# Kernel optimization log

Measured on AMD Instinct MI355X. Metric: run time of the kernel, lower is better.

The kernel has to match this reference:

```python
import jax, jax.numpy as jnp
import numpy as np

DIM = 512
NUM_HEADS = 16
WINDOW_SIZE = 32
POS_HIDDEN = DIM // 4  # int(dim // mlp_ratio) with mlp_ratio=4.0


def _window_partition(coords, window_size):
    # coords: (B, N, 3) -> window ids (B, N)
    B, N, _ = coords.shape
    cmin = coords.min(axis=1, keepdims=True)
    cmax = coords.max(axis=1, keepdims=True)
    crange = cmax - cmin
    crange = jnp.where(crange < 1e-6, jnp.ones_like(crange), crange)
    cnorm = (coords - cmin) / crange
    grid_res = max(1, round((N / window_size) ** (1.0 / 3.0)))  # static Python int
    bin_idx = jnp.clip((cnorm * grid_res).astype(jnp.int32), 0, grid_res - 1)
    window_id = bin_idx[..., 0] * (grid_res * grid_res) + bin_idx[..., 1] * grid_res + bin_idx[..., 2]
    return window_id


def setup_inputs() -> dict:
    key = jax.random.key(0)
    ks = jax.random.split(key, 10)
    B, N, C = 2, 1024, DIM
    s = 0.02
    return {
        "coords": jax.random.uniform(ks[0], (B, N, 3), dtype=jnp.float32),
        "x": jax.random.normal(ks[1], (B, N, C), dtype=jnp.float32),
        "qkv_w": jax.random.normal(ks[2], (3 * C, C), dtype=jnp.float32) * s,
        "qkv_b": jnp.zeros((3 * C,), dtype=jnp.float32),
        "proj_w": jax.random.normal(ks[3], (C, C), dtype=jnp.float32) * s,
        "proj_b": jnp.zeros((C,), dtype=jnp.float32),
        "pos_w1": jax.random.normal(ks[4], (POS_HIDDEN, 3), dtype=jnp.float32) * 0.1,
        "pos_b1": jnp.zeros((POS_HIDDEN,), dtype=jnp.float32),
        "pos_w2": jax.random.normal(ks[5], (NUM_HEADS, POS_HIDDEN), dtype=jnp.float32) * 0.1,
        "pos_b2": jnp.zeros((NUM_HEADS,), dtype=jnp.float32),
    }


def reference(coords, x, qkv_w, qkv_b, proj_w, proj_b, pos_w1, pos_b1, pos_w2, pos_b2):
    B, N, C = x.shape
    H = NUM_HEADS
    D = C // H
    # QKV projection
    qkv = x @ qkv_w.T + qkv_b  # (B, N, 3C)
    q, k, v = jnp.split(qkv, 3, axis=-1)
    q = q.reshape(B, N, H, D).transpose(0, 2, 1, 3)  # (B, H, N, D)
    k = k.reshape(B, N, H, D).transpose(0, 2, 1, 3)
    v = v.reshape(B, N, H, D).transpose(0, 2, 1, 3)
    window_id = _window_partition(coords, WINDOW_SIZE)  # (B, N)
    scale = D ** (-0.5)
    attn = jnp.einsum("bhnd,bhmd->bhnm", q, k) * scale  # (B, H, N, N)
    # per-pair MLP relative position bias (exact GELU, matching torch nn.GELU)
    offsets = coords[:, :, None, :] - coords[:, None, :, :]  # (B, N, N, 3)
    hid = jax.nn.gelu(offsets @ pos_w1.T + pos_b1, approximate=False)
    rel_pos_bias = hid @ pos_w2.T + pos_b2  # (B, N, N, H)
    attn = attn + rel_pos_bias.transpose(0, 3, 1, 2)
    # window mask: masked_fill with -10000.0 for cross-window pairs
    same_window = (window_id[:, :, None] == window_id[:, None, :])[:, None]  # (B,1,N,N)
    attn = jnp.where(same_window, attn, jnp.float32(-10000.0))
    attn = jax.nn.softmax(attn, axis=-1)
    out = jnp.einsum("bhnm,bhmd->bhnd", attn, v)
    out = out.transpose(0, 2, 1, 3).reshape(B, N, C)
    return out @ proj_w.T + proj_b
```

## Files before the change

### kernel.cpp

```cpp
#include <hip/hip_runtime.h>
#include <hip/hip_bf16.h>
#include <math.h>

#define B_  2
#define N_  1024
#define C_  512
#define H_  16
#define D_  32
#define NW  27
#define NWT (B_*NW)
#define CAPP 98304
#define GEMM_BLKS 768
#define BIAS_BLKS 512

typedef __attribute__((ext_vector_type(8))) short short8;
typedef __attribute__((ext_vector_type(4))) short short4e;
typedef __attribute__((ext_vector_type(4))) float f32x4;

__device__ __forceinline__ ushort f2bf(float x){
  unsigned u = __float_as_uint(x);
  return (ushort)((u + 0x7fffu + ((u>>16)&1u)) >> 16);
}
__device__ __forceinline__ float bf2f(ushort b){
  return __uint_as_float(((unsigned)b)<<16);
}

#define GLL16(gptr, lptr) __builtin_amdgcn_global_load_lds( \
    (const __attribute__((address_space(1))) void*)(gptr),  \
    (__attribute__((address_space(3))) void*)(lptr), 16, 0, 0)

__device__ __forceinline__ float gelu_exact(float t){
  const float y = t*0.70710678118654752f;
  const float u = y*y;
  float E;
  if (u < 0.5f) {
    float q =           -7.5757576e-4f;
    q = fmaf(q,u,  4.6296297e-3f);
    q = fmaf(q,u, -2.3809524e-2f);
    q = fmaf(q,u,  0.1f);
    q = fmaf(q,u, -0.33333334f);
    q = fmaf(q,u,  1.0f);
    E = 1.1283791671f * y * q;
  } else {
    E = erff(y);
  }
  return 0.5f*t*(1.0f + E);
}

__global__ __launch_bounds__(1024) void winprep_kernel(
    const float* __restrict__ coords,
    int* __restrict__ counts, int* __restrict__ offsets, int* __restrict__ sidx,
    const float* __restrict__ x, const float* __restrict__ qkv_w,
    const float* __restrict__ proj_w, const float* __restrict__ pw2,
    const float* __restrict__ pw1, const float* __restrict__ pb1,
    ushort* __restrict__ Xh, ushort* __restrict__ Xl,
    ushort* __restrict__ Wqh, ushort* __restrict__ Wql,
    ushort* __restrict__ Wph, ushort* __restrict__ Wpl,
    ushort* __restrict__ W2bh, ushort* __restrict__ W2bl,
    float4* __restrict__ w14)
{
  const int bid = blockIdx.x;
  if (bid < 2) {
    const int b = bid;
    const int i = threadIdx.x;
    const int lane = i & 63, wv = i >> 6;
    const float c0 = coords[(b*N_+i)*3+0];
    const float c1 = coords[(b*N_+i)*3+1];
    const float c2 = coords[(b*N_+i)*3+2];
    float mn0=c0,mx0=c0,mn1=c1,mx1=c1,mn2=c2,mx2=c2;
    #pragma unroll
    for (int o=32;o>=1;o>>=1) {
      mn0=fminf(mn0,__shfl_xor(mn0,o)); mx0=fmaxf(mx0,__shfl_xor(mx0,o));
      mn1=fminf(mn1,__shfl_xor(mn1,o)); mx1=fmaxf(mx1,__shfl_xor(mx1,o));
      mn2=fminf(mn2,__shfl_xor(mn2,o)); mx2=fmaxf(mx2,__shfl_xor(mx2,o));
    }
    __shared__ float red[16][6];
    __shared__ float bmin[3], rng[3];
    __shared__ int wavecnt[16][NW];
    __shared__ int waveoff[16][NW];
    __shared__ int wcnt[NW], woff[NW];
    if (lane==0){ red[wv][0]=mn0;red[wv][1]=mn1;red[wv][2]=mn2;red[wv][3]=mx0;red[wv][4]=mx1;red[wv][5]=mx2; }
    __syncthreads();
    if (i==0){
      float a0=red[0][0],a1=red[0][1],a2=red[0][2];
      float d0=red[0][3],d1=red[0][4],d2=red[0][5];
      for (int t=1;t<16;++t){
        a0=fminf(a0,red[t][0]); a1=fminf(a1,red[t][1]); a2=fminf(a2,red[t][2]);
        d0=fmaxf(d0,red[t][3]); d1=fmaxf(d1,red[t][4]); d2=fmaxf(d2,red[t][5]);
      }
      bmin[0]=a0;bmin[1]=a1;bmin[2]=a2;
      float r0=d0-a0, r1=d1-a1, r2=d2-a2;
      rng[0]=(r0<1e-6f)?1.f:r0; rng[1]=(r1<1e-6f)?1.f:r1; rng[2]=(r2<1e-6f)?1.f:r2;
    }
    __syncthreads();
    int bx=(int)(((c0-bmin[0])/rng[0])*3.0f); bx=min(max(bx,0),2);
    int by=(int)(((c1-bmin[1])/rng[1])*3.0f); by=min(max(by,0),2);
    int bz=(int)(((c2-bmin[2])/rng[2])*3.0f); bz=min(max(bz,0),2);
    const int wid = bx*9+by*3+bz;
    unsigned long long mymask=0ull;
    for (int w=0;w<NW;++w){
      unsigned long long m = __ballot(wid==w);
      if (w==wid) mymask=m;
      if (lane==0) wavecnt[wv][w]=(int)__popcll(m);
    }
    __syncthreads();
    if (i<NW){ int s=0; for(int t=0;t<16;++t) s+=wavecnt[t][i]; wcnt[i]=s; }
    __syncthreads();
    if (i==0){ int r=0; for(int w=0;w<NW;++w){ woff[w]=r; r+=wcnt[w]; } }
    __syncthreads();
    if (i<NW){ int o=woff[i]; for(int t=0;t<16;++t){ waveoff[t][i]=o; o+=wavecnt[t][i]; } }
    __syncthreads();
    const int rank = waveoff[wv][wid] + (int)__popcll(mymask & ((1ull<<lane)-1ull));
    sidx[b*N_ + rank] = i;
    if (i<NW){ counts[b*NW+i]=wcnt[i]; offsets[b*NW+i]=woff[i]; }
    return;
  }
  const int gid = (bid - 2)*1024 + threadIdx.x;
  if (bid == 2 && threadIdx.x < 128) {
    const int u = threadIdx.x;
    w14[u] = make_float4(pw1[u*3+0], pw1[u*3+1], pw1[u*3+2], pb1[u]);
  }
  if (gid >= 262400) return;
  const float* src; ushort* ph; ushort* pl; int i;
  if (gid < 131072)      { src = x;      ph = Xh;   pl = Xl;   i = gid; }
  else if (gid < 229376) { src = qkv_w;  ph = Wqh;  pl = Wql;  i = gid - 131072; }
  else if (gid < 262144) { src = proj_w; ph = Wph;  pl = Wpl;  i = gid - 229376; }
  else                   { src = pw2;    ph = W2bh; pl = W2bl; i = gid - 262144; }
  const float4 a = ((const float4*)src)[i*2+0];
  const float4 b = ((const float4*)src)[i*2+1];
  const float v[8] = {a.x,a.y,a.z,a.w,b.x,b.y,b.z,b.w};
  ushort hv[8], lv[8];
  #pragma unroll
  for (int t=0;t<8;++t){ hv[t]=f2bf(v[t]); lv[t]=f2bf(v[t]-bf2f(hv[t])); }
  ((ushort4*)ph)[i*2+0] = make_ushort4(hv[0],hv[1],hv[2],hv[3]);
  ((ushort4*)ph)[i*2+1] = make_ushort4(hv[4],hv[5],hv[6],hv[7]);
  ((ushort4*)pl)[i*2+0] = make_ushort4(lv[0],lv[1],lv[2],lv[3]);
  ((ushort4*)pl)[i*2+1] = make_ushort4(lv[4],lv[5],lv[6],lv[7]);
}

__global__ __launch_bounds__(256) void gemm_bias_kernel(
    const ushort* __restrict__ Ah, const ushort* __restrict__ Al,
    const ushort* __restrict__ Bh, const ushort* __restrict__ Bl,
    const float* __restrict__ bias,
    ushort* __restrict__ Yh, ushort* __restrict__ Yl,
    const float* __restrict__ coords, const float4* __restrict__ w14,
    const ushort* __restrict__ W2bh, const ushort* __restrict__ W2bl,
    const float* __restrict__ pb2,
    const int* __restrict__ counts, const int* __restrict__ offsets,
    const int* __restrict__ sidx, float* __restrict__ bias_ws)
{
  __shared__ __align__(16) char smem[32768];
  const int tid = threadIdx.x;
  const int bid = blockIdx.x;

  if (bid < GEMM_BLKS) {
    ushort* lds = (ushort*)smem;
    const int wv = tid >> 6, lane = tid & 63;
    const int bm = (bid & 31)*64, bn = (bid >> 5)*64;
    const int wm = wv >> 1, wn = wv & 1;
    const int r15 = lane & 15, qq = lane >> 4;
    const int srow8 = lane >> 3, sg = lane & 7;
    const int qr = sg ^ srow8;
    const int K = 512, Nd = 1536;

    f32x4 acc[2][2];
    #pragma unroll
    for (int i=0;i<2;++i)
      #pragma unroll
      for (int j=0;j<2;++j)
        #pragma unroll
        for (int r=0;r<4;++r) acc[i][j][r]=0.f;

    const ushort* gT[4] = {Ah, Al, Bh, Bl};
    const ushort* gMy = gT[wv];
    const int tb = (wv < 2) ? bm : bn;

    for (int k0 = 0; k0 < K; k0 += 64) {
      __syncthreads();
      #pragma unroll
      for (int c=0;c<8;++c)
        GLL16(gMy + (size_t)(tb + c*8 + srow8)*K + k0 + qr*8, &lds[wv*4096 + c*512]);
      __syncthreads();

      #pragma unroll
      for (int kk=0; kk<2; ++kk) {
        short8 ah[2], al[2], bh[2], bl[2];
        #pragma unroll
        for (int mi=0; mi<2; ++mi){
          const int row = wm*32 + mi*16 + r15;
          const int s = ((kk*4+qq) ^ (row&7))*8;
          ah[mi] = *(const short8*)&lds[0    + row*64 + s];
          al[mi] = *(const short8*)&lds[4096 + row*64 + s];
        }
        #pragma unroll
        for (int nj=0; nj<2; ++nj){
          const int row = wn*32 + nj*16 + r15;
          const int s = ((kk*4+qq) ^ (row&7))*8;
          bh[nj] = *(const short8*)&lds[8192  + row*64 + s];
          bl[nj] = *(const short8*)&lds[12288 + row*64 + s];
        }
        #pragma unroll
        for (int mi=0; mi<2; ++mi)
          #pragma unroll
          for (int nj=0; nj<2; ++nj){
            acc[mi][nj] = __builtin_amdgcn_mfma_f32_16x16x32_bf16(ah[mi], bh[nj], acc[mi][nj], 0,0,0);
            acc[mi][nj] = __builtin_amdgcn_mfma_f32_16x16x32_bf16(ah[mi], bl[nj], acc[mi][nj], 0,0,0);
            acc[mi][nj] = __builtin_amdgcn_mfma_f32_16x16x32_bf16(al[mi], bh[nj], acc[mi][nj], 0,0,0);
          }
      }
    }
    #pragma unroll
    for (int mi=0;mi<2;++mi){
      const int gr0 = bm + wm*32 + mi*16 + qq*4;
      #pragma unroll
      for (int nj=0;nj<2;++nj){
        const int gc = bn + wn*32 + nj*16 + r15;
        const float bb = bias[gc];
        #pragma unroll
        for (int r=0;r<4;++r){
          const float v = acc[mi][nj][r] + bb;
          const ushort hh = f2bf(v);
          Yh[(size_t)(gr0+r)*Nd + gc] = hh;
          Yl[(size_t)(gr0+r)*Nd + gc] = f2bf(v - bf2f(hh));
        }
      }
    }
    return;
  }

  ushort* sGh  = (ushort*)smem;
  ushort* sGl  = (ushort*)(smem + 8704);
  ushort* sW2h = (ushort*)(smem + 17408);
  ushort* sW2l = (ushort*)(smem + 21760);
  float4* sW1T = (float4*)(smem + 26112);
  int* s_n   = (int*)(smem + 28288);
  int* s_end = (int*)(smem + 28544);
  int* s_off = (int*)(smem + 28800);

  if (tid < 128) sW1T[(tid&7)*17 + (tid>>3)] = w14[tid];
  {
    const int head = tid >> 4, u0 = (tid & 15)*8;
    *(ushort4*)&sW2h[head*136 + u0]     = *(const ushort4*)&W2bh[head*128 + u0];
    *(ushort4*)&sW2h[head*136 + u0 + 4] = *(const ushort4*)&W2bh[head*128 + u0 + 4];
    *(ushort4*)&sW2l[head*136 + u0]     = *(const ushort4*)&W2bl[head*128 + u0];
    *(ushort4*)&sW2l[head*136 + u0 + 4] = *(const ushort4*)&W2bl[head*128 + u0 + 4];
  }
  if (tid < 64) {
    const int cnt = (tid < NWT) ? counts[tid] : 0;
    s_n[tid] = cnt;
    s_off[tid] = (tid < NWT) ? (tid/NW)*N_ + offsets[tid] : 0;
    int v = cnt*cnt;
    #pragma unroll
    for (int o=1;o<64;o<<=1){ const int t2=__shfl_up(v,o); if (tid>=o) v+=t2; }
    s_end[tid] = v;
  }
  __syncthreads();
  const int total_pairs = s_end[NWT-1];
  const int nchunks = (total_pairs + 31) >> 5;

  const int wv = tid >> 6, lane = tid & 63;
  const int r15 = lane & 15, qq = lane >> 4;
  const float pb = pb2[r15];

  for (int ch = bid - GEMM_BLKS; ch < nchunks; ch += BIAS_BLKS) {
    const int pair0 = ch*32;
    {
      const int p = tid >> 3, e = tid & 7;
      const int pair = pair0 + p;
      if (pair < total_pairs) {
        int lo = 0, hi = NWT;
        #pragma unroll
        for (int it=0; it<6; ++it) {
          const int mid = (lo + hi) >> 1;
          if (lo < hi) { if (s_end[mid] <= pair) lo = mid + 1; else hi = mid; }
        }
        const int w = lo;
        const int n  = s_n[w];
        const int pp = pair - (s_end[w] - n*n);
        const unsigned q = (unsigned)pp / (unsigned)n;
        const int k  = pp - (int)q*n;
        const int off = s_off[w];
        const int b  = w / NW;
        const int qg = sidx[off + q];
        const int kg = sidx[off + k];
        const float ox = coords[(b*N_+qg)*3+0] - coords[(b*N_+kg)*3+0];
        const float oy = coords[(b*N_+qg)*3+1] - coords[(b*N_+kg)*3+1];
        const float oz = coords[(b*N_+qg)*3+2] - coords[(b*N_+kg)*3+2];
        #pragma unroll 1
        for (int jj=0; jj<4; ++jj) {
          float gv[4];
          #pragma unroll
          for (int r=0;r<4;++r) {
            const int u = e*16 + jj*4 + r;
            const float4 wvv = sW1T[(u&7)*17 + (u>>3)];
            const float t = fmaf(ox,wvv.x, fmaf(oy,wvv.y, fmaf(oz,wvv.z, wvv.w)));
            gv[r] = gelu_exact(t);
          }
          ushort h0=f2bf(gv[0]), h1=f2bf(gv[1]), h2=f2bf(gv[2]), h3=f2bf(gv[3]);
          *(ushort4*)&sGh[p*136 + e*16 + jj*4] = make_ushort4(h0,h1,h2,h3);
          *(ushort4*)&sGl[p*136 + e*16 + jj*4] = make_ushort4(
              f2bf(gv[0]-bf2f(h0)), f2bf(gv[1]-bf2f(h1)),
              f2bf(gv[2]-bf2f(h2)), f2bf(gv[3]-bf2f(h3)));
        }
      }
    }
    __syncthreads();
    if (wv < 2) {
      const int tb = wv*16;
      f32x4 acc;
      #pragma unroll
      for (int r=0;r<4;++r) acc[r]=0.f;
      #pragma unroll
      for (int kk=0; kk<4; ++kk) {
        const int ko = kk*32 + qq*8;
        const short8 gh = *(const short8*)&sGh[(tb+r15)*136 + ko];
        const short8 gl = *(const short8*)&sGl[(tb+r15)*136 + ko];
        const short8 wh = *(const short8*)&sW2h[r15*136 + ko];
        const short8 wl = *(const short8*)&sW2l[r15*136 + ko];
        acc = __builtin_amdgcn_mfma_f32_16x16x32_bf16(gh, wh, acc, 0,0,0);
        acc = __builtin_amdgcn_mfma_f32_16x16x32_bf16(gh, wl, acc, 0,0,0);
        acc = __builtin_amdgcn_mfma_f32_16x16x32_bf16(gl, wh, acc, 0,0,0);
      }
      #pragma unroll
      for (int r=0;r<4;++r) {
        const int pair = pair0 + tb + qq*4 + r;
        if (pair < total_pairs)
          bias_ws[(size_t)r15*CAPP + pair] = acc[r] + pb;
      }
    }
    __syncthreads();
  }
}

__global__ __launch_bounds__(256) void gemm_mfma(
    const ushort* __restrict__ Ah, const ushort* __restrict__ Al,
    const ushort* __restrict__ Bh, const ushort* __restrict__ Bl,
    const float* __restrict__ bias, float* __restrict__ Y,
    const int Nd, const int K)
{
  __shared__ ushort lds[8192];
  const int tid = threadIdx.x;
  const int wv = tid >> 6, lane = tid & 63;
  const int bm = blockIdx.x*32, bn = blockIdx.y*32;
  const int wm = wv >> 1, wn = wv & 1;
  const int r15 = lane & 15, qq = lane >> 4;
  const int srow8 = lane >> 3, sg = lane & 7;
  const int qr = sg ^ srow8;

  f32x4 acc;
  #pragma unroll
  for (int r=0;r<4;++r) acc[r]=0.f;

  const ushort* gT[4] = {Ah, Al, Bh, Bl};
  const ushort* gMy = gT[wv];
  const int tb = (wv < 2) ? bm : bn;

  for (int k0 = 0; k0 < K; k0 += 64) {
    __syncthreads();
    #pragma unroll
    for (int c=0;c<4;++c)
      GLL16(gMy + (size_t)(tb + c*8 + srow8)*K + k0 + qr*8, &lds[wv*2048 + c*512]);
    __syncthreads();

    #pragma unroll
    for (int kk=0; kk<2; ++kk) {
      const int rowa = wm*16 + r15;
      const int sa = ((kk*4+qq) ^ (rowa&7))*8;
      const short8 ah = *(const short8*)&lds[0    + rowa*64 + sa];
      const short8 al = *(const short8*)&lds[2048 + rowa*64 + sa];
      const int rowb = wn*16 + r15;
      const int sb = ((kk*4+qq) ^ (rowb&7))*8;
      const short8 bh = *(const short8*)&lds[4096 + rowb*64 + sb];
      const short8 bl = *(const short8*)&lds[6144 + rowb*64 + sb];
      acc = __builtin_amdgcn_mfma_f32_16x16x32_bf16(ah, bh, acc, 0,0,0);
      acc = __builtin_amdgcn_mfma_f32_16x16x32_bf16(ah, bl, acc, 0,0,0);
      acc = __builtin_amdgcn_mfma_f32_16x16x32_bf16(al, bh, acc, 0,0,0);
    }
  }
  const int gr0 = bm + wm*16 + qq*4;
  const int gc  = bn + wn*16 + r15;
  const float bb = bias[gc];
  #pragma unroll
  for (int r=0;r<4;++r)
    Y[(size_t)(gr0+r)*Nd + gc] = acc[r] + bb;
}

__global__ __launch_bounds__(256) void attn3_kernel(
    const ushort* __restrict__ Qh_, const ushort* __restrict__ Ql_,
    const float* __restrict__ bias_ws,
    const int* __restrict__ counts, const int* __restrict__ offsets,
    const int* __restrict__ sidx,
    ushort* __restrict__ aout_h, ushort* __restrict__ aout_l)
{
  const int bwi = blockIdx.x;
  const int b = bwi / NW;
  const int n = counts[bwi];
  const int q0 = blockIdx.y * 16;
  if (q0 >= n) return;
  const int hg = blockIdx.z;
  const int off = b*N_ + offsets[bwi];
  const int tid = threadIdx.x;
  const int wv = tid >> 6, lane = tid & 63;
  const int r15 = lane & 15, qq = lane >> 4;
  const int h = hg*4 + wv;

  __shared__ __align__(16) ushort sPh[4][16*36];
  __shared__ __align__(16) ushort sPl[4][16*36];
  __shared__ __align__(16) ushort sVh[4][32*36];
  __shared__ __align__(16) ushort sVl[4][32*36];
  __shared__ int s_qidx[16];
  __shared__ int s_pb;

  if (tid < 64) {
    const int cnt = (tid < NWT) ? counts[tid] : 0;
    int v = cnt*cnt;
    #pragma unroll
    for (int o=1;o<64;o<<=1){ const int t2=__shfl_up(v,o); if (tid>=o) v+=t2; }
    if (tid == bwi) s_pb = v - cnt*cnt;
  }
  const int qn = min(16, n - q0);
  if (tid < 16) s_qidx[tid] = sidx[off + q0 + ((tid < qn) ? tid : 0)];
  for (int t = lane; t < 256; t += 64) {
    const int row = t >> 4, col = 16 + (t & 15);
    sPh[wv][row*36 + col] = 0; sPl[wv][row*36 + col] = 0;
  }
  for (int t = lane; t < 512; t += 64) {
    const int row = t >> 4, col = 16 + (t & 15);
    sVh[wv][row*36 + col] = 0; sVl[wv][row*36 + col] = 0;
  }
  __syncthreads();
  const int pbase = s_pb;
  const float* biasP = bias_ws + (size_t)h*CAPP + pbase;

  const size_t qrow = ((size_t)(b*N_ + s_qidx[r15]))*1536 + h*32 + qq*8;
  const short8 qfh = *(const short8*)(Qh_ + qrow);
  const short8 qfl = *(const short8*)(Ql_ + qrow);

  const float scale = 0.17677669529663687f;
  float mrun[4] = {-1e30f,-1e30f,-1e30f,-1e30f};
  float lrun[4] = {0.f,0.f,0.f,0.f};
  f32x4 accO[2];
  #pragma unroll
  for (int half=0; half<2; ++half)
    #pragma unroll
    for (int r=0;r<4;++r) accO[half][r]=0.f;

  for (int kc0 = 0; kc0 < n; kc0 += 16) {
    const int kn = min(16, n - kc0);
    const int kg = sidx[off + kc0 + ((r15 < kn) ? r15 : 0)];
    const size_t krow = ((size_t)(b*N_ + kg))*1536 + 512 + h*32 + qq*8;
    const short8 kfh = *(const short8*)(Qh_ + krow);
    const short8 kfl = *(const short8*)(Ql_ + krow);
    f32x4 s;
    #pragma unroll
    for (int r=0;r<4;++r) s[r]=0.f;
    s = __builtin_amdgcn_mfma_f32_16x16x32_bf16(qfh, kfh, s, 0,0,0);
    s = __builtin_amdgcn_mfma_f32_16x16x32_bf16(qfh, kfl, s, 0,0,0);
    s = __builtin_amdgcn_mfma_f32_16x16x32_bf16(qfl, kfh, s, 0,0,0);
    const short8 vfh = *(const short8*)(Qh_ + krow + 512);
    const short8 vfl = *(const short8*)(Ql_ + krow + 512);
    #pragma unroll
    for (int j=0;j<8;++j){
      const int d = qq*8 + j;
      sVh[wv][d*36 + r15] = (ushort)vfh[j];
      sVl[wv][d*36 + r15] = (ushort)vfl[j];
    }
    float p[4], sc[4];
    #pragma unroll
    for (int r=0;r<4;++r){
      const int row = qq*4 + r;
      float sv;
      if (row < qn && r15 < kn)
        sv = fmaf(s[r], scale, biasP[(q0+row)*n + kc0 + r15]);
      else
        sv = -1e30f;
      float tm = sv;
      #pragma unroll
      for (int o=1;o<16;o<<=1) tm = fmaxf(tm, __shfl_xor(tm, o));
      const float mn = fmaxf(mrun[r], tm);
      sc[r] = __expf(mrun[r] - mn);
      p[r]  = __expf(sv - mn);
      float ls = p[r];
      #pragma unroll
      for (int o=1;o<16;o<<=1) ls += __shfl_xor(ls, o);
      lrun[r] = lrun[r]*sc[r] + ls;
      mrun[r] = mn;
    }
    #pragma unroll
    for (int half=0; half<2; ++half)
      #pragma unroll
      for (int r=0;r<4;++r) accO[half][r] *= sc[r];
    #pragma unroll
    for (int r=0;r<4;++r){
      const int row = qq*4 + r;
      const ushort ph = f2bf(p[r]);
      sPh[wv][row*36 + r15] = ph;
      sPl[wv][row*36 + r15] = f2bf(p[r] - bf2f(ph));
    }
    {
      const int pb0 = r15*36 + qq*8;
      const short4e pl0h = *(const short4e*)&sPh[wv][pb0];
      const short4e pl1h = *(const short4e*)&sPh[wv][pb0 + 4];
      const short4e pl0l = *(const short4e*)&sPl[wv][pb0];
      const short4e pl1l = *(const short4e*)&sPl[wv][pb0 + 4];
      short8 pah, pal;
      pah[0]=pl0h[0]; pah[1]=pl0h[1]; pah[2]=pl0h[2]; pah[3]=pl0h[3];
      pah[4]=pl1h[0]; pah[5]=pl1h[1]; pah[6]=pl1h[2]; pah[7]=pl1h[3];
      pal[0]=pl0l[0]; pal[1]=pl0l[1]; pal[2]=pl0l[2]; pal[3]=pl0l[3];
      pal[4]=pl1l[0]; pal[5]=pl1l[1]; pal[6]=pl1l[2]; pal[7]=pl1l[3];
      #pragma unroll
      for (int half=0; half<2; ++half){
        const int vb0 = (half*16 + r15)*36 + qq*8;
        const short4e vl0h = *(const short4e*)&sVh[wv][vb0];
        const short4e vl1h = *(const short4e*)&sVh[wv][vb0 + 4];
        const short4e vl0l = *(const short4e*)&sVl[wv][vb0];
        const short4e vl1l = *(const short4e*)&sVl[wv][vb0 + 4];
        short8 vbh, vbl;
        vbh[0]=vl0h[0]; vbh[1]=vl0h[1]; vbh[2]=vl0h[2]; vbh[3]=vl0h[3];
        vbh[4]=vl1h[0]; vbh[5]=vl1h[1]; vbh[6]=vl1h[2]; vbh[7]=vl1h[3];
        vbl[0]=vl0l[0]; vbl[1]=vl0l[1]; vbl[2]=vl0l[2]; vbl[3]=vl0l[3];
        vbl[4]=vl1l[0]; vbl[5]=vl1l[1]; vbl[6]=vl1l[2]; vbl[7]=vl1l[3];
        accO[half] = __builtin_amdgcn_mfma_f32_16x16x32_bf16(pah, vbh, accO[half], 0,0,0);
        accO[half] = __builtin_amdgcn_mfma_f32_16x16x32_bf16(pah, vbl, accO[half], 0,0,0);
        accO[half] = __builtin_amdgcn_mfma_f32_16x16x32_bf16(pal, vbh, accO[half], 0,0,0);
      }
    }
  }
  #pragma unroll
  for (int r=0;r<4;++r){
    const int row = qq*4 + r;
    if (row < qn) {
      const float inv = 1.0f / lrun[r];
      const size_t ob = ((size_t)(b*N_ + s_qidx[row]))*C_ + h*32;
      #pragma unroll
      for (int half=0; half<2; ++half){
        const float v = accO[half][r] * inv;
        const ushort hh = f2bf(v);
        aout_h[ob + half*16 + r15] = hh;
        aout_l[ob + half*16 + r15] = f2bf(v - bf2f(hh));
      }
    }
  }
}

extern "C" void kernel_launch(void* const* d_in, const int* in_sizes, int n_in,
                              void* d_out, int out_size, void* d_ws, size_t ws_size,
                              hipStream_t stream)
{
  const float* coords = (const float*)d_in[0];
  const float* x      = (const float*)d_in[1];
  const float* qkv_w  = (const float*)d_in[2];
  const float* qkv_b  = (const float*)d_in[3];
  const float* proj_w = (const float*)d_in[4];
  const float* proj_b = (const float*)d_in[5];
  const float* pw1    = (const float*)d_in[6];
  const float* pb1    = (const float*)d_in[7];
  const float* pw2    = (const float*)d_in[8];
  const float* pb2    = (const float*)d_in[9];
  float* out = (float*)d_out;

  ushort* Qkvh     = (ushort*)d_ws;
  ushort* Qkvl     = Qkvh + (size_t)2048*1536;
  float*  bias_ws  = (float*)(Qkvl + (size_t)2048*1536);
  float4* w14      = (float4*)(bias_ws + (size_t)16*CAPP);
  int*    counts   = (int*)(w14 + 128);
  int*    offsets  = counts + 64;
  int*    sidx     = offsets + 64;
  ushort* Xh       = (ushort*)(sidx + 2048);
  ushort* Xl       = Xh + (size_t)2048*512;
  ushort* Wqh      = Xl + (size_t)2048*512;
  ushort* Wql      = Wqh + (size_t)1536*512;
  ushort* Wph      = Wql + (size_t)1536*512;
  ushort* Wpl      = Wph + (size_t)512*512;
  ushort* W2bh     = Wpl + (size_t)512*512;
  ushort* W2bl     = W2bh + 2048;

  hipLaunchKernelGGL(winprep_kernel, dim3(259), dim3(1024), 0, stream,
                     coords, counts, offsets, sidx,
                     x, qkv_w, proj_w, pw2, pw1, pb1,
                     Xh, Xl, Wqh, Wql, Wph, Wpl, W2bh, W2bl, w14);
  hipLaunchKernelGGL(gemm_bias_kernel, dim3(GEMM_BLKS + BIAS_BLKS), dim3(256), 0, stream,
                     Xh, Xl, Wqh, Wql, qkv_b, Qkvh, Qkvl,
                     coords, w14, W2bh, W2bl, pb2, counts, offsets, sidx, bias_ws);
  hipLaunchKernelGGL(attn3_kernel, dim3(NWT, 8, 4), dim3(256), 0, stream,
                     Qkvh, Qkvl, bias_ws, counts, offsets, sidx, Xh, Xl);
  hipLaunchKernelGGL(gemm_mfma,   dim3(64,16), dim3(256),  0, stream,
                     Xh, Xl, Wph, Wpl, proj_b, out, 512, 512);
}
```

Measured before the change: 69.39 us.

## Scatter QKV GEMM output into window-sorted per-head layout for attention

The QKV GEMM epilogue now writes each row to its window-sorted rank in a per-(q/k/v, head) contiguous buffer of 32-wide rows, using a rank array produced by the window-prep kernel. The attention kernel then reads Q, K and V contiguously by sorted position instead of gathering through sidx with a 1536-element row stride. This removes the indirect index load and the scattered 64-byte gathers in the inner attention loop. In exchange the GEMM stores become scattered 2-byte writes across 48 planes, and the kernel relies on sorted K rows past the window end being in bounds (padding via PS).

```diff
diff --git a/kernel.cpp b/kernel.cpp
--- a/kernel.cpp
+++ b/kernel.cpp
@@ -12,6 +12,7 @@
 #define CAPP 98304
 #define GEMM_BLKS 768
 #define BIAS_BLKS 512
+#define PS 66048
 
 typedef __attribute__((ext_vector_type(8))) short short8;
 typedef __attribute__((ext_vector_type(4))) short short4e;
@@ -50,6 +51,7 @@
 __global__ __launch_bounds__(1024) void winprep_kernel(
     const float* __restrict__ coords,
     int* __restrict__ counts, int* __restrict__ offsets, int* __restrict__ sidx,
+    int* __restrict__ rank_arr,
     const float* __restrict__ x, const float* __restrict__ qkv_w,
     const float* __restrict__ proj_w, const float* __restrict__ pw2,
     const float* __restrict__ pw1, const float* __restrict__ pb1,
@@ -112,6 +114,7 @@
     __syncthreads();
     const int rank = waveoff[wv][wid] + (int)__popcll(mymask & ((1ull<<lane)-1ull));
     sidx[b*N_ + rank] = i;
+    rank_arr[b*N_ + i] = b*N_ + rank;
     if (i<NW){ counts[b*NW+i]=wcnt[i]; offsets[b*NW+i]=woff[i]; }
     return;
   }
@@ -142,7 +145,8 @@
     const ushort* __restrict__ Ah, const ushort* __restrict__ Al,
     const ushort* __restrict__ Bh, const ushort* __restrict__ Bl,
     const float* __restrict__ bias,
-    ushort* __restrict__ Yh, ushort* __restrict__ Yl,
+    ushort* __restrict__ Tsh, ushort* __restrict__ Tsl,
+    const int* __restrict__ rank_arr,
     const float* __restrict__ coords, const float4* __restrict__ w14,
     const ushort* __restrict__ W2bh, const ushort* __restrict__ W2bl,
     const float* __restrict__ pb2,
@@ -161,7 +165,7 @@
     const int r15 = lane & 15, qq = lane >> 4;
     const int srow8 = lane >> 3, sg = lane & 7;
     const int qr = sg ^ srow8;
-    const int K = 512, Nd = 1536;
+    const int K = 512;
 
     f32x4 acc[2][2];
     #pragma unroll
@@ -209,19 +213,29 @@
           }
       }
     }
+    int srow_[2][4];
+    #pragma unroll
+    for (int mi=0;mi<2;++mi)
+      #pragma unroll
+      for (int r=0;r<4;++r)
+        srow_[mi][r] = rank_arr[bm + wm*32 + mi*16 + qq*4 + r];
     #pragma unroll
     for (int mi=0;mi<2;++mi){
-      const int gr0 = bm + wm*32 + mi*16 + qq*4;
       #pragma unroll
       for (int nj=0;nj<2;++nj){
-        const int gc = bn + wn*32 + nj*16 + r15;
-        const float bb = bias[gc];
+        const int gcb  = bn + wn*32 + nj*16;
+        const int kind = gcb >> 9;
+        const int hd   = (gcb >> 5) & 15;
+        const int d    = (gcb & 31) + r15;
+        const size_t pbase = (size_t)(kind*16 + hd)*PS;
+        const float bb = bias[gcb + r15];
         #pragma unroll
         for (int r=0;r<4;++r){
           const float v = acc[mi][nj][r] + bb;
           const ushort hh = f2bf(v);
-          Yh[(size_t)(gr0+r)*Nd + gc] = hh;
-          Yl[(size_t)(gr0+r)*Nd + gc] = f2bf(v - bf2f(hh));
+          const size_t a2 = pbase + (size_t)srow_[mi][r]*32 + d;
+          Tsh[a2] = hh;
+          Tsl[a2] = f2bf(v - bf2f(hh));
         }
       }
     }
@@ -386,7 +400,7 @@
 }
 
 __global__ __launch_bounds__(256) void attn3_kernel(
-    const ushort* __restrict__ Qh_, const ushort* __restrict__ Ql_,
+    const ushort* __restrict__ Tsh, const ushort* __restrict__ Tsl,
     const float* __restrict__ bias_ws,
     const int* __restrict__ counts, const int* __restrict__ offsets,
     const int* __restrict__ sidx,
@@ -432,9 +446,16 @@
   const int pbase = s_pb;
   const float* biasP = bias_ws + (size_t)h*CAPP + pbase;
 
-  const size_t qrow = ((size_t)(b*N_ + s_qidx[r15]))*1536 + h*32 + qq*8;
-  const short8 qfh = *(const short8*)(Qh_ + qrow);
-  const short8 qfl = *(const short8*)(Ql_ + qrow);
+  const ushort* Qh = Tsh + (size_t)h*PS;
+  const ushort* Ql = Tsl + (size_t)h*PS;
+  const ushort* Kh = Tsh + (size_t)(16 + h)*PS;
+  const ushort* Kl = Tsl + (size_t)(16 + h)*PS;
+  const ushort* Vh = Tsh + (size_t)(32 + h)*PS;
+  const ushort* Vl = Tsl + (size_t)(32 + h)*PS;
+
+  const int qi = (off + q0 + r15)*32 + qq*8;
+  const short8 qfh = *(const short8*)(Qh + qi);
+  const short8 qfl = *(const short8*)(Ql + qi);
 
   const float scale = 0.17677669529663687f;
   float mrun[4] = {-1e30f,-1e30f,-1e30f,-1e30f};
@@ -447,18 +468,17 @@
 
   for (int kc0 = 0; kc0 < n; kc0 += 16) {
     const int kn = min(16, n - kc0);
-    const int kg = sidx[off + kc0 + ((r15 < kn) ? r15 : 0)];
-    const size_t krow = ((size_t)(b*N_ + kg))*1536 + 512 + h*32 + qq*8;
-    const short8 kfh = *(const short8*)(Qh_ + krow);
-    const short8 kfl = *(const short8*)(Ql_ + krow);
+    const int ki = (off + kc0 + r15)*32 + qq*8;
+    const short8 kfh = *(const short8*)(Kh + ki);
+    const short8 kfl = *(const short8*)(Kl + ki);
     f32x4 s;
     #pragma unroll
     for (int r=0;r<4;++r) s[r]=0.f;
     s = __builtin_amdgcn_mfma_f32_16x16x32_bf16(qfh, kfh, s, 0,0,0);
     s = __builtin_amdgcn_mfma_f32_16x16x32_bf16(qfh, kfl, s, 0,0,0);
     s = __builtin_amdgcn_mfma_f32_16x16x32_bf16(qfl, kfh, s, 0,0,0);
-    const short8 vfh = *(const short8*)(Qh_ + krow + 512);
-    const short8 vfl = *(const short8*)(Ql_ + krow + 512);
+    const short8 vfh = *(const short8*)(Vh + ki);
+    const short8 vfl = *(const short8*)(Vl + ki);
     #pragma unroll
     for (int j=0;j<8;++j){
       const int d = qq*8 + j;
@@ -559,14 +579,15 @@
   const float* pb2    = (const float*)d_in[9];
   float* out = (float*)d_out;
 
-  ushort* Qkvh     = (ushort*)d_ws;
-  ushort* Qkvl     = Qkvh + (size_t)2048*1536;
-  float*  bias_ws  = (float*)(Qkvl + (size_t)2048*1536);
+  ushort* Tsh      = (ushort*)d_ws;
+  ushort* Tsl      = Tsh + (size_t)48*PS;
+  float*  bias_ws  = (float*)(Tsl + (size_t)48*PS);
   float4* w14      = (float4*)(bias_ws + (size_t)16*CAPP);
   int*    counts   = (int*)(w14 + 128);
   int*    offsets  = counts + 64;
   int*    sidx     = offsets + 64;
-  ushort* Xh       = (ushort*)(sidx + 2048);
+  int*    rank_arr = sidx + 2048;
+  ushort* Xh       = (ushort*)(rank_arr + 2048);
   ushort* Xl       = Xh + (size_t)2048*512;
   ushort* Wqh      = Xl + (size_t)2048*512;
   ushort* Wql      = Wqh + (size_t)1536*512;
@@ -576,14 +597,14 @@
   ushort* W2bl     = W2bh + 2048;
 
   hipLaunchKernelGGL(winprep_kernel, dim3(259), dim3(1024), 0, stream,
-                     coords, counts, offsets, sidx,
+                     coords, counts, offsets, sidx, rank_arr,
                      x, qkv_w, proj_w, pw2, pw1, pb1,
                      Xh, Xl, Wqh, Wql, Wph, Wpl, W2bh, W2bl, w14);
   hipLaunchKernelGGL(gemm_bias_kernel, dim3(GEMM_BLKS + BIAS_BLKS), dim3(256), 0, stream,
-                     Xh, Xl, Wqh, Wql, qkv_b, Qkvh, Qkvl,
+                     Xh, Xl, Wqh, Wql, qkv_b, Tsh, Tsl, rank_arr,
                      coords, w14, W2bh, W2bl, pb2, counts, offsets, sidx, bias_ws);
   hipLaunchKernelGGL(attn3_kernel, dim3(NWT, 8, 4), dim3(256), 0, stream,
-                     Qkvh, Qkvl, bias_ws, counts, offsets, sidx, Xh, Xl);
+                     Tsh, Tsl, bias_ws, counts, offsets, sidx, Xh, Xl);
   hipLaunchKernelGGL(gemm_mfma,   dim3(64,16), dim3(256),  0, stream,
                      Xh, Xl, Wph, Wpl, proj_b, out, 512, 512);
 }
```

Result: no change. 68.21 us (-1.7%).
